# Performance work log

Measured on AMD Instinct MI355X. Metric: run time of the kernel, lower is better.

Reference implementation:

```python
import jax, jax.numpy as jnp
import numpy as np

N = 100000
E = 1000000
IN, HID, OUT = 128, 64, 40


def setup_inputs() -> dict:
    key = jax.random.key(0)
    k1, k2, k3, k4 = jax.random.split(key, 4)
    x = jax.random.normal(k1, (N, IN), dtype=jnp.float32)
    edge_index = jax.random.randint(k2, (2, E), 0, N, dtype=jnp.int64)
    W1 = jax.random.normal(k3, (IN, HID), dtype=jnp.float32) * (1.0 / np.sqrt(IN))
    b1 = jnp.zeros((HID,), dtype=jnp.float32)
    W2 = jax.random.normal(k4, (HID, OUT), dtype=jnp.float32) * (1.0 / np.sqrt(HID))
    b2 = jnp.zeros((OUT,), dtype=jnp.float32)
    return {"x": x, "edge_index": edge_index, "W1": W1, "b1": b1, "W2": W2, "b2": b2}


def _gcn_norm(edge_index, num_nodes):
    # PyG GCNConv default: add self-loops, symmetric normalization deg^-1/2 A deg^-1/2
    loop = jnp.arange(num_nodes, dtype=edge_index.dtype)
    src = jnp.concatenate([edge_index[0], loop])
    dst = jnp.concatenate([edge_index[1], loop])
    deg = jax.ops.segment_sum(jnp.ones_like(dst, dtype=jnp.float32), dst, num_segments=num_nodes)
    dinv = jnp.where(deg > 0, jax.lax.rsqrt(deg), 0.0)
    norm = dinv[src] * dinv[dst]  # [E+N]
    return src, dst, norm


def _gcn_conv(h, W, b, src, dst, norm, num_nodes):
    h = h @ W                          # [N, d_out] dense transform
    msg = h[src] * norm[:, None]       # gather + scale per edge
    out = jax.ops.segment_sum(msg, dst, num_segments=num_nodes)  # scatter-add
    return out + b


def reference(x, edge_index, W1, b1, W2, b2):
    src, dst, norm = _gcn_norm(edge_index, N)
    h = jax.nn.relu(_gcn_conv(x, W1, b1, src, dst, norm, N))
    # dropout is identity at inference (module in eval mode)
    out = _gcn_conv(h, W2, b2, src, dst, norm, N)
    return out
```

## Files before the change

kernel.cpp:

```cpp
#include <hip/hip_runtime.h>

#define NN 100000
#define EE 1000000
#define IN_F 128
#define HID_F 64
#define OUT_F 40
#define BUCKET 48
#define BIN_NODES 256
#define NBINS 391
#define FIFO_CAP 4096
#define P1_CHUNK 4096
#define P1_BUF 32

typedef _Float16 half8 __attribute__((ext_vector_type(8)));
typedef _Float16 half4 __attribute__((ext_vector_type(4)));
typedef float f32x4 __attribute__((ext_vector_type(4)));

#define SWZ(b, row) ((b) ^ (((row) & 7) << 4))

static __device__ __forceinline__ int atomic_add_i32(int* p, int v) {
    return __hip_atomic_fetch_add(p, v, __ATOMIC_RELAXED, __HIP_MEMORY_SCOPE_AGENT);
}

static __device__ __forceinline__ f32x4 h4f4(half4 h) {
    f32x4 r = {(float)h.x, (float)h.y, (float)h.z, (float)h.w};
    return r;
}

__global__ __launch_bounds__(256) void k_prep(const float* __restrict__ W1,
                                              const float* __restrict__ W2,
                                              _Float16* __restrict__ w1t,
                                              _Float16* __restrict__ w2t,
                                              int* __restrict__ bincur) {
    int i = blockIdx.x * 256 + threadIdx.x;
    if (i < IN_F * HID_F) {
        int k = i >> 6, n = i & 63;
        w1t[n * IN_F + k] = (_Float16)W1[i];
    }
    if (i < 48 * HID_F) {
        int n = i >> 6, k = i & 63;
        w2t[i] = (_Float16)((n < OUT_F) ? W2[k * OUT_F + n] : 0.f);
    }
    if (i < NBINS) bincur[i] = 0;
}

__global__ __launch_bounds__(256) void k_bin(const int* __restrict__ ei,
                                             int* __restrict__ bincur,
                                             unsigned* __restrict__ fifo) {
    __shared__ unsigned buf[NBINS][P1_BUF];
    __shared__ int lcnt[NBINS];
    __shared__ int lbase[NBINS];
    const int tid = threadIdx.x;
    for (int j = tid; j < NBINS; j += 256) lcnt[j] = 0;
    __syncthreads();

    const int e0 = blockIdx.x * P1_CHUNK;
    #pragma unroll
    for (int i = 0; i < P1_CHUNK / 256; ++i) {
        int e = e0 + i * 256 + tid;
        if (e < EE) {
            int s = ei[e];
            int d = ei[EE + e];
            int bin = d >> 8;
            unsigned pk = ((unsigned)s << 8) | (unsigned)(d & 255);
            int p = atomicAdd(&lcnt[bin], 1);
            if (p < P1_BUF) {
                buf[bin][p] = pk;
            } else {
                int gp = atomic_add_i32(&bincur[bin], 1);
                if (gp < FIFO_CAP) fifo[(size_t)bin * FIFO_CAP + gp] = pk;
            }
        }
    }
    __syncthreads();
    for (int j = tid; j < NBINS; j += 256) {
        int cnt = lcnt[j]; if (cnt > P1_BUF) cnt = P1_BUF;
        lbase[j] = (cnt > 0) ? atomic_add_i32(&bincur[j], cnt) : 0;
        lcnt[j] = cnt;
    }
    __syncthreads();
    for (int j = tid; j < NBINS; j += 256) {
        int cnt = lcnt[j];
        int base = lbase[j];
        for (int k = 0; k < cnt; ++k) {
            int gp = base + k;
            if (gp < FIFO_CAP) fifo[(size_t)j * FIFO_CAP + gp] = buf[j][k];
        }
    }
}

__global__ __launch_bounds__(256) void k_csr(const int* __restrict__ bincur,
                                             const unsigned* __restrict__ fifo,
                                             int* __restrict__ csr,
                                             int* __restrict__ deg,
                                             float* __restrict__ dinv) {
    __shared__ int cur[BIN_NODES];
    __shared__ int stage[BIN_NODES * BUCKET];
    const int tid = threadIdx.x;
    const int bin = blockIdx.x;
    const int v0 = bin * BIN_NODES;
    const int nnode = (NN - v0 < BIN_NODES) ? (NN - v0) : BIN_NODES;
    if (tid < BIN_NODES) cur[tid] = 0;
    __syncthreads();

    int cnt = bincur[bin]; if (cnt > FIFO_CAP) cnt = FIFO_CAP;
    for (int k = tid; k < cnt; k += 256) {
        unsigned u = fifo[(size_t)bin * FIFO_CAP + k];
        int dl = u & 255;
        int s = (int)(u >> 8);
        int p = atomicAdd(&cur[dl], 1);
        if (p < BUCKET) stage[dl * BUCKET + p] = s;
    }
    __syncthreads();

    const int total = nnode * BUCKET;
    for (int idx = tid; idx < total; idx += 256)
        csr[(size_t)v0 * BUCKET + idx] = stage[idx];
    if (tid < nnode) {
        int d = cur[tid];
        deg[v0 + tid] = d;
        dinv[v0 + tid] = rsqrtf((float)(d + 1));
    }
}

__global__ __launch_bounds__(256) void k_gemm1(const float* __restrict__ x,
                                               const _Float16* __restrict__ w1t,
                                               const float* __restrict__ dinv,
                                               _Float16* __restrict__ h1s) {
    __shared__ _Float16 As[64 * IN_F];
    __shared__ _Float16 Bs[64 * IN_F];
    const int tid = threadIdx.x;
    const size_t r0 = (size_t)blockIdx.x * 64;

    #pragma unroll
    for (int i = 0; i < 8; ++i) {
        int f = i * 256 + tid;
        int row = f >> 5;
        int k4 = (f & 31) * 4;
        size_t gr = r0 + row; if (gr >= NN) gr = NN - 1;
        float4 v = *(const float4*)&x[gr * IN_F + k4];
        _Float16 h[4] = {(_Float16)v.x, (_Float16)v.y, (_Float16)v.z, (_Float16)v.w};
        *(uint2*)((char*)As + SWZ(row * 256 + k4 * 2, row)) = *(uint2*)h;
    }
    #pragma unroll
    for (int i = 0; i < 4; ++i) {
        int c = i * 256 + tid;
        int col = c >> 4;
        int k8 = (c & 15) * 8;
        uint4 v = *(const uint4*)&w1t[col * IN_F + k8];
        *(uint4*)((char*)Bs + SWZ(col * 256 + k8 * 2, col)) = v;
    }
    __syncthreads();

    const int w = tid >> 6, l = tid & 63;
    const int lr = l & 15, lg = l >> 4;
    const int R0 = w * 16;
    f32x4 acc[4] = {};
    #pragma unroll
    for (int kk = 0; kk < 4; ++kk) {
        const int kbyte = (kk * 32 + lg * 8) * 2;
        const int arow = R0 + lr;
        half8 a = *(const half8*)((const char*)As + SWZ(arow * 256 + kbyte, arow));
        #pragma unroll
        for (int t = 0; t < 4; ++t) {
            const int bcol = t * 16 + lr;
            half8 b = *(const half8*)((const char*)Bs + SWZ(bcol * 256 + kbyte, bcol));
            acc[t] = __builtin_amdgcn_mfma_f32_16x16x32_f16(a, b, acc[t], 0, 0, 0);
        }
    }
    #pragma unroll
    for (int r = 0; r < 4; ++r) {
        size_t row = r0 + R0 + lg * 4 + r;
        if (row < NN) {
            float dv = dinv[row];
            #pragma unroll
            for (int t = 0; t < 4; ++t)
                h1s[row * HID_F + t * 16 + lr] = (_Float16)(dv * acc[t][r]);
        }
    }
}

__global__ __launch_bounds__(256) void k_agg1(const _Float16* __restrict__ h1s,
                                              const float* __restrict__ dinv,
                                              const int* __restrict__ degA,
                                              const int* __restrict__ csr,
                                              const float* __restrict__ b1,
                                              _Float16* __restrict__ hrelu) {
    const int tid = threadIdx.x;
    const int v = blockIdx.x * 16 + (tid >> 4);
    if (v >= NN) return;
    const int c = tid & 15;
    const size_t base = (size_t)v << 6;

    int deg = degA[v];
    if (deg > BUCKET) deg = BUCKET;
    const int start = v * BUCKET;
    const int end = start + deg;

    f32x4 accA = h4f4(*(const half4*)&h1s[base + c * 4]);
    f32x4 accB = {};
    int t = start;
    for (; t + 3 < end; t += 4) {
        int4 s4 = *(const int4*)&csr[t];
        half4 a0 = *(const half4*)&h1s[((size_t)s4.x << 6) + c * 4];
        half4 a1 = *(const half4*)&h1s[((size_t)s4.y << 6) + c * 4];
        half4 a2 = *(const half4*)&h1s[((size_t)s4.z << 6) + c * 4];
        half4 a3 = *(const half4*)&h1s[((size_t)s4.w << 6) + c * 4];
        accA += h4f4(a0); accB += h4f4(a1); accA += h4f4(a2); accB += h4f4(a3);
    }
    for (; t < end; ++t)
        accA += h4f4(*(const half4*)&h1s[((size_t)csr[t] << 6) + c * 4]);
    accA += accB;

    const float dv = dinv[v];
    float4 bb = *(const float4*)&b1[c * 4];
    _Float16 o[4];
    o[0] = (_Float16)fmaxf(dv * accA[0] + bb.x, 0.f);
    o[1] = (_Float16)fmaxf(dv * accA[1] + bb.y, 0.f);
    o[2] = (_Float16)fmaxf(dv * accA[2] + bb.z, 0.f);
    o[3] = (_Float16)fmaxf(dv * accA[3] + bb.w, 0.f);
    *(uint2*)&hrelu[base + c * 4] = *(uint2*)o;
}

__global__ __launch_bounds__(256) void k_gemm2(const _Float16* __restrict__ hr,
                                               const _Float16* __restrict__ w2t,
                                               const float* __restrict__ dinv,
                                               _Float16* __restrict__ tabA,
                                               _Float16* __restrict__ tabB) {
    __shared__ _Float16 As[64 * HID_F];
    __shared__ _Float16 Bs[48 * HID_F];
    const int tid = threadIdx.x;
    const size_t r0 = (size_t)blockIdx.x * 64;

    #pragma unroll
    for (int i = 0; i < 2; ++i) {
        int c = i * 256 + tid;
        int row = c >> 3;
        int k8 = (c & 7) * 8;
        size_t gr = r0 + row; if (gr >= NN) gr = NN - 1;
        uint4 v = *(const uint4*)&hr[gr * HID_F + k8];
        *(uint4*)((char*)As + SWZ(row * 128 + k8 * 2, row)) = v;
    }
    for (int c = tid; c < 384; c += 256) {
        int col = c >> 3;
        int k8 = (c & 7) * 8;
        uint4 v = *(const uint4*)&w2t[col * HID_F + k8];
        *(uint4*)((char*)Bs + SWZ(col * 128 + k8 * 2, col)) = v;
    }
    __syncthreads();

    const int w = tid >> 6, l = tid & 63;
    const int lr = l & 15, lg = l >> 4;
    const int R0 = w * 16;
    f32x4 acc[3] = {};
    #pragma unroll
    for (int kk = 0; kk < 2; ++kk) {
        const int kbyte = (kk * 32 + lg * 8) * 2;
        const int arow = R0 + lr;
        half8 a = *(const half8*)((const char*)As + SWZ(arow * 128 + kbyte, arow));
        #pragma unroll
        for (int t = 0; t < 3; ++t) {
            const int bcol = t * 16 + lr;
            half8 b = *(const half8*)((const char*)Bs + SWZ(bcol * 128 + kbyte, bcol));
            acc[t] = __builtin_amdgcn_mfma_f32_16x16x32_f16(a, b, acc[t], 0, 0, 0);
        }
    }
    #pragma unroll
    for (int r = 0; r < 4; ++r) {
        size_t row = r0 + R0 + lg * 4 + r;
        if (row < NN) {
            float dv = dinv[row];
            #pragma unroll
            for (int t = 0; t < 3; ++t) {
                int col = t * 16 + lr;
                float val = dv * acc[t][r];
                if (col < 32) tabA[row * 32 + col] = (_Float16)val;
                else if (col < OUT_F) tabB[row * 8 + (col - 32)] = (_Float16)val;
            }
        }
    }
}

__global__ __launch_bounds__(256) void k_agg2(const _Float16* __restrict__ tabA,
                                              const _Float16* __restrict__ tabB,
                                              const float* __restrict__ dinv,
                                              const int* __restrict__ degA,
                                              const int* __restrict__ csr,
                                              const float* __restrict__ b2,
                                              float* __restrict__ out) {
    const int tid = threadIdx.x;
    const int v = blockIdx.x * 16 + (tid >> 4);
    if (v >= NN) return;
    const int c = tid & 15;
    const bool useA = (c < 8);
    const size_t aoff = useA ? (size_t)c * 4 : 0;
    const size_t boff = (c >= 8 && c < 10) ? (size_t)(c - 8) * 4 : 0;

    int deg = degA[v];
    if (deg > BUCKET) deg = BUCKET;
    const int start = v * BUCKET;
    const int end = start + deg;

    f32x4 accA, accB = {};
    {
        const _Float16* p = useA ? tabA + ((size_t)v << 5) + aoff : tabB + ((size_t)v << 3) + boff;
        accA = h4f4(*(const half4*)p);
    }
    int t = start;
    for (; t + 3 < end; t += 4) {
        int4 s4 = *(const int4*)&csr[t];
        const _Float16* p0 = useA ? tabA + ((size_t)s4.x << 5) + aoff : tabB + ((size_t)s4.x << 3) + boff;
        const _Float16* p1 = useA ? tabA + ((size_t)s4.y << 5) + aoff : tabB + ((size_t)s4.y << 3) + boff;
        const _Float16* p2 = useA ? tabA + ((size_t)s4.z << 5) + aoff : tabB + ((size_t)s4.z << 3) + boff;
        const _Float16* p3 = useA ? tabA + ((size_t)s4.w << 5) + aoff : tabB + ((size_t)s4.w << 3) + boff;
        half4 a0 = *(const half4*)p0;
        half4 a1 = *(const half4*)p1;
        half4 a2 = *(const half4*)p2;
        half4 a3 = *(const half4*)p3;
        accA += h4f4(a0); accB += h4f4(a1); accA += h4f4(a2); accB += h4f4(a3);
    }
    for (; t < end; ++t) {
        int s0 = csr[t];
        const _Float16* p0 = useA ? tabA + ((size_t)s0 << 5) + aoff : tabB + ((size_t)s0 << 3) + boff;
        accA += h4f4(*(const half4*)p0);
    }
    accA += accB;

    if (c < 10) {
        const float dv = dinv[v];
        float4 bb = *(const float4*)&b2[c * 4];
        float4 o = {dv * accA[0] + bb.x, dv * accA[1] + bb.y,
                    dv * accA[2] + bb.z, dv * accA[3] + bb.w};
        *(float4*)&out[(size_t)v * OUT_F + c * 4] = o;
    }
}

extern "C" void kernel_launch(void* const* d_in, const int* in_sizes, int n_in,
                              void* d_out, int out_size, void* d_ws, size_t ws_size,
                              hipStream_t stream) {
    const float* x  = (const float*)d_in[0];
    const int*   ei = (const int*)d_in[1];
    const float* W1 = (const float*)d_in[2];
    const float* b1 = (const float*)d_in[3];
    const float* W2 = (const float*)d_in[4];
    const float* b2 = (const float*)d_in[5];
    float* out = (float*)d_out;

    char* p = (char*)d_ws;
    float*     dinv   = (float*)p;     p += (size_t)NN * 4;
    int*       deg    = (int*)p;       p += (size_t)NN * 4;
    int*       bincur = (int*)p;       p += 512 * 4;
    unsigned*  fifo   = (unsigned*)p;  p += (size_t)NBINS * FIFO_CAP * 4;
    _Float16*  w1t    = (_Float16*)p;  p += (size_t)IN_F * HID_F * 2;
    _Float16*  w2t    = (_Float16*)p;  p += (size_t)48 * HID_F * 2;
    int*       csr    = (int*)p;       p += (size_t)NN * BUCKET * 4;
    _Float16*  h1s    = (_Float16*)p;  p += (size_t)NN * HID_F * 2;
    _Float16*  hrelu  = (_Float16*)p;  p += (size_t)NN * HID_F * 2;
    _Float16*  tabA   = (_Float16*)p;  p += (size_t)NN * 32 * 2;
    _Float16*  tabB   = (_Float16*)p;  p += ((size_t)NN * 8 + 32) * 2;

    const int gemm_blocks = (NN + 63) / 64;
    const int agg_blocks = (NN + 15) / 16;
    const int bin_blocks = (EE + P1_CHUNK - 1) / P1_CHUNK;

    k_prep <<<32, 256, 0, stream>>>(W1, W2, w1t, w2t, bincur);
    k_bin  <<<bin_blocks, 256, 0, stream>>>(ei, bincur, fifo);
    k_csr  <<<NBINS, 256, 0, stream>>>(bincur, fifo, csr, deg, dinv);
    k_gemm1<<<gemm_blocks, 256, 0, stream>>>(x, w1t, dinv, h1s);
    k_agg1 <<<agg_blocks, 256, 0, stream>>>(h1s, dinv, deg, csr, b1, hrelu);
    k_gemm2<<<gemm_blocks, 256, 0, stream>>>(hrelu, w2t, dinv, tabA, tabB);
    k_agg2 <<<agg_blocks, 256, 0, stream>>>(tabA, tabB, dinv, deg, csr, b2, out);
}
```

Baseline: 111.0 us.

## Fuse layer-1 aggregation into second GEMM and vectorize CSR store

```diff
diff --git a/kernel.cpp b/kernel.cpp
--- a/kernel.cpp
+++ b/kernel.cpp
@@ -9,8 +9,8 @@
 #define BIN_NODES 256
 #define NBINS 391
 #define FIFO_CAP 4096
-#define P1_CHUNK 4096
-#define P1_BUF 32
+#define P1_CHUNK 2048
+#define P1_BUF 16
 
 typedef _Float16 half8 __attribute__((ext_vector_type(8)));
 typedef _Float16 half4 __attribute__((ext_vector_type(4)));
@@ -113,9 +113,10 @@
     }
     __syncthreads();
 
-    const int total = nnode * BUCKET;
-    for (int idx = tid; idx < total; idx += 256)
-        csr[(size_t)v0 * BUCKET + idx] = stage[idx];
+    const int total4 = nnode * BUCKET / 4;
+    int4* dst4 = (int4*)&csr[(size_t)v0 * BUCKET];
+    for (int idx = tid; idx < total4; idx += 256)
+        dst4[idx] = *(const int4*)&stage[idx * 4];
     if (tid < nnode) {
         int d = cur[tid];
         deg[v0 + tid] = d;
@@ -180,72 +181,63 @@
     }
 }
 
-__global__ __launch_bounds__(256) void k_agg1(const _Float16* __restrict__ h1s,
-                                              const float* __restrict__ dinv,
-                                              const int* __restrict__ degA,
-                                              const int* __restrict__ csr,
-                                              const float* __restrict__ b1,
-                                              _Float16* __restrict__ hrelu) {
-    const int tid = threadIdx.x;
-    const int v = blockIdx.x * 16 + (tid >> 4);
-    if (v >= NN) return;
-    const int c = tid & 15;
-    const size_t base = (size_t)v << 6;
-
-    int deg = degA[v];
-    if (deg > BUCKET) deg = BUCKET;
-    const int start = v * BUCKET;
-    const int end = start + deg;
-
-    f32x4 accA = h4f4(*(const half4*)&h1s[base + c * 4]);
-    f32x4 accB = {};
-    int t = start;
-    for (; t + 3 < end; t += 4) {
-        int4 s4 = *(const int4*)&csr[t];
-        half4 a0 = *(const half4*)&h1s[((size_t)s4.x << 6) + c * 4];
-        half4 a1 = *(const half4*)&h1s[((size_t)s4.y << 6) + c * 4];
-        half4 a2 = *(const half4*)&h1s[((size_t)s4.z << 6) + c * 4];
-        half4 a3 = *(const half4*)&h1s[((size_t)s4.w << 6) + c * 4];
-        accA += h4f4(a0); accB += h4f4(a1); accA += h4f4(a2); accB += h4f4(a3);
-    }
-    for (; t < end; ++t)
-        accA += h4f4(*(const half4*)&h1s[((size_t)csr[t] << 6) + c * 4]);
-    accA += accB;
-
-    const float dv = dinv[v];
-    float4 bb = *(const float4*)&b1[c * 4];
-    _Float16 o[4];
-    o[0] = (_Float16)fmaxf(dv * accA[0] + bb.x, 0.f);
-    o[1] = (_Float16)fmaxf(dv * accA[1] + bb.y, 0.f);
-    o[2] = (_Float16)fmaxf(dv * accA[2] + bb.z, 0.f);
-    o[3] = (_Float16)fmaxf(dv * accA[3] + bb.w, 0.f);
-    *(uint2*)&hrelu[base + c * 4] = *(uint2*)o;
-}
-
-__global__ __launch_bounds__(256) void k_gemm2(const _Float16* __restrict__ hr,
-                                               const _Float16* __restrict__ w2t,
-                                               const float* __restrict__ dinv,
-                                               _Float16* __restrict__ tabA,
-                                               _Float16* __restrict__ tabB) {
+__global__ __launch_bounds__(256) void k_agg1g2(const _Float16* __restrict__ h1s,
+                                                const float* __restrict__ dinv,
+                                                const int* __restrict__ degA,
+                                                const int* __restrict__ csr,
+                                                const float* __restrict__ b1,
+                                                const _Float16* __restrict__ w2t,
+                                                _Float16* __restrict__ tabA,
+                                                _Float16* __restrict__ tabB) {
     __shared__ _Float16 As[64 * HID_F];
     __shared__ _Float16 Bs[48 * HID_F];
     const int tid = threadIdx.x;
     const size_t r0 = (size_t)blockIdx.x * 64;
 
-    #pragma unroll
-    for (int i = 0; i < 2; ++i) {
-        int c = i * 256 + tid;
-        int row = c >> 3;
-        int k8 = (c & 7) * 8;
-        size_t gr = r0 + row; if (gr >= NN) gr = NN - 1;
-        uint4 v = *(const uint4*)&hr[gr * HID_F + k8];
-        *(uint4*)((char*)As + SWZ(row * 128 + k8 * 2, row)) = v;
-    }
-    for (int c = tid; c < 384; c += 256) {
-        int col = c >> 3;
-        int k8 = (c & 7) * 8;
-        uint4 v = *(const uint4*)&w2t[col * HID_F + k8];
-        *(uint4*)((char*)Bs + SWZ(col * 128 + k8 * 2, col)) = v;
+    for (int cB = tid; cB < 384; cB += 256) {
+        int col = cB >> 3;
+        int k8 = (cB & 7) * 8;
+        uint4 vB = *(const uint4*)&w2t[col * HID_F + k8];
+        *(uint4*)((char*)Bs + SWZ(col * 128 + k8 * 2, col)) = vB;
+    }
+
+    const int grp = tid >> 4;
+    const int c = tid & 15;
+    float4 bb = *(const float4*)&b1[c * 4];
+    #pragma unroll
+    for (int i = 0; i < 4; ++i) {
+        const int row = grp + i * 16;
+        const size_t v = r0 + row;
+        if (v >= NN) continue;
+        const size_t base = v << 6;
+
+        int dg = degA[v];
+        if (dg > BUCKET) dg = BUCKET;
+        const int start = (int)v * BUCKET;
+        const int end = start + dg;
+
+        f32x4 accA = h4f4(*(const half4*)&h1s[base + c * 4]);
+        f32x4 accB = {};
+        int t = start;
+        for (; t + 3 < end; t += 4) {
+            int4 s4 = *(const int4*)&csr[t];
+            half4 a0 = *(const half4*)&h1s[((size_t)s4.x << 6) + c * 4];
+            half4 a1 = *(const half4*)&h1s[((size_t)s4.y << 6) + c * 4];
+            half4 a2 = *(const half4*)&h1s[((size_t)s4.z << 6) + c * 4];
+            half4 a3 = *(const half4*)&h1s[((size_t)s4.w << 6) + c * 4];
+            accA += h4f4(a0); accB += h4f4(a1); accA += h4f4(a2); accB += h4f4(a3);
+        }
+        for (; t < end; ++t)
+            accA += h4f4(*(const half4*)&h1s[((size_t)csr[t] << 6) + c * 4]);
+        accA += accB;
+
+        const float dv = dinv[v];
+        _Float16 o[4];
+        o[0] = (_Float16)fmaxf(dv * accA[0] + bb.x, 0.f);
+        o[1] = (_Float16)fmaxf(dv * accA[1] + bb.y, 0.f);
+        o[2] = (_Float16)fmaxf(dv * accA[2] + bb.z, 0.f);
+        o[3] = (_Float16)fmaxf(dv * accA[3] + bb.w, 0.f);
+        *(uint2*)((char*)As + SWZ(row * 128 + c * 8, row)) = *(uint2*)o;
     }
     __syncthreads();
 
@@ -355,19 +347,17 @@
     _Float16*  w2t    = (_Float16*)p;  p += (size_t)48 * HID_F * 2;
     int*       csr    = (int*)p;       p += (size_t)NN * BUCKET * 4;
     _Float16*  h1s    = (_Float16*)p;  p += (size_t)NN * HID_F * 2;
-    _Float16*  hrelu  = (_Float16*)p;  p += (size_t)NN * HID_F * 2;
     _Float16*  tabA   = (_Float16*)p;  p += (size_t)NN * 32 * 2;
     _Float16*  tabB   = (_Float16*)p;  p += ((size_t)NN * 8 + 32) * 2;
 
     const int gemm_blocks = (NN + 63) / 64;
-    const int agg_blocks = (NN + 15) / 16;
+    const int agg2_blocks = (NN + 15) / 16;
     const int bin_blocks = (EE + P1_CHUNK - 1) / P1_CHUNK;
 
-    k_prep <<<32, 256, 0, stream>>>(W1, W2, w1t, w2t, bincur);
-    k_bin  <<<bin_blocks, 256, 0, stream>>>(ei, bincur, fifo);
-    k_csr  <<<NBINS, 256, 0, stream>>>(bincur, fifo, csr, deg, dinv);
-    k_gemm1<<<gemm_blocks, 256, 0, stream>>>(x, w1t, dinv, h1s);
-    k_agg1 <<<agg_blocks, 256, 0, stream>>>(h1s, dinv, deg, csr, b1, hrelu);
-    k_gemm2<<<gemm_blocks, 256, 0, stream>>>(hrelu, w2t, dinv, tabA, tabB);
-    k_agg2 <<<agg_blocks, 256, 0, stream>>>(tabA, tabB, dinv, deg, csr, b2, out);
-}
+    k_prep  <<<32, 256, 0, stream>>>(W1, W2, w1t, w2t, bincur);
+    k_bin   <<<bin_blocks, 256, 0, stream>>>(ei, bincur, fifo);
+    k_csr   <<<NBINS, 256, 0, stream>>>(bincur, fifo, csr, deg, dinv);
+    k_gemm1 <<<gemm_blocks, 256, 0, stream>>>(x, w1t, dinv, h1s);
+    k_agg1g2<<<gemm_blocks, 256, 0, stream>>>(h1s, dinv, deg, csr, b1, w2t, tabA, tabB);
+    k_agg2  <<<agg2_blocks, 256, 0, stream>>>(tabA, tabB, dinv, deg, csr, b2, out);
+}
```

Result: faster. 107.9 us (-2.8%).
